# Optimization experiments

Hardware: AMD Instinct MI355X
Metric: run time of the kernel (lower is better)

## Reference

```python
import jax, jax.numpy as jnp
import numpy as np

B, T, Q, H = 128, 50, 1024, 256
MAX_STEP = 50
TEMP = 0.5
SUP_W, DIST_W, EMBED_W, LOSS_WEIGHT = 1.0, 0.01, 1.0, 1.0
BLUR, DIAMETER, REACH, SCALING, P = 0.005, 1.0, 500.0, 0.5, 2
NEG = -1e9


def _softmin(eps, C, h):
    # h: log-weights + potential/eps over the second axis of C
    return -eps * jax.nn.logsumexp(h[None, :] - C / eps, axis=1)


def _sqcost(u, v):
    sq = jnp.sum(u * u, -1)[:, None] + jnp.sum(v * v, -1)[None, :] - 2.0 * (u @ v.T)
    return 0.5 * jnp.maximum(sq, 0.0)  # geomloss p=2 cost: |x-y|^2 / 2


def sinkhorn_divergence(x, y):
    # geomloss SamplesLoss('sinkhorn', p=2, blur=0.005, diameter=1, reach=500),
    # tensorized, debiased, unbalanced, eps-scaling schedule.
    N, M = x.shape[0], y.shape[0]
    a_log = jnp.full((N,), -np.log(float(N)), dtype=x.dtype)
    b_log = jnp.full((M,), -np.log(float(M)), dtype=x.dtype)
    Cxy, Cyx = _sqcost(x, y), _sqcost(y, x)
    Cxx, Cyy = _sqcost(x, x), _sqcost(y, y)
    rho = REACH ** P
    eps_final = BLUR ** P
    eps_list = []
    e = DIAMETER ** P
    while e > eps_final:
        eps_list.append(e)
        e = e * (SCALING ** P)
    eps_list.append(eps_final)
    f_ab = jnp.zeros((N,), x.dtype)
    g_ab = jnp.zeros((M,), x.dtype)
    f_aa = jnp.zeros((N,), x.dtype)
    g_bb = jnp.zeros((M,), x.dtype)
    for eps in eps_list:  # static schedule (~9 steps)
        damp = 1.0 / (1.0 + eps / rho)
        ft = damp * _softmin(eps, Cxy, b_log + g_ab / eps)
        gt = damp * _softmin(eps, Cyx, a_log + f_ab / eps)
        faa = 0.5 * (f_aa + damp * _softmin(eps, Cxx, a_log + f_aa / eps))
        gbb = 0.5 * (g_bb + damp * _softmin(eps, Cyy, b_log + g_bb / eps))
        f_ab, g_ab, f_aa, g_bb = ft, gt, faa, gbb
    w = rho + eps_final / 2.0  # UnbalancedWeight
    a_w, b_w = jnp.exp(a_log), jnp.exp(b_log)
    return (jnp.sum(a_w * w * (jnp.exp(-f_aa / rho) - jnp.exp(-f_ab / rho)))
            + jnp.sum(b_w * w * (jnp.exp(-g_bb / rho) - jnp.exp(-g_ab / rho))))


def _forward(lc, lt, le, ltc, ltt, lte, ohs, oht, ods, odt, batch):
    p_c, p_t, p_e = lc / TEMP, lt / TEMP, le / TEMP
    q_c, q_t, q_e = ltc / TEMP, ltt / TEMP, lte / TEMP
    flat = lambda z: z.reshape(z.shape[0], -1)
    loss_kd = (sinkhorn_divergence(flat(p_c), flat(q_c))
               + sinkhorn_divergence(flat(p_t), flat(q_t))
               + sinkhorn_divergence(flat(p_e), flat(q_e)))
    S = MAX_STEP - 1
    delta = batch[:, :, :Q] + batch[:, :, Q:]  # [B,T,Q] question one-hots
    a = jnp.floor(((batch[:, :, :Q] - batch[:, :, Q:]).sum(-1) + 1.0) / 2.0)[:, 1:1 + S]  # [B,S] correctness
    dsh = delta[:, 1:1 + S]  # [B,S,Q]
    # diagonal of p[:S] @ delta[1:].T == per-step gather of next question's logit
    pc = jnp.einsum('bsq,bsq->bs', p_c[:, :S], dsh)
    pt = jnp.einsum('bsq,bsq->bs', p_t[:, :S], dsh)
    pe = jnp.einsum('bsq,bsq->bs', p_e[:, :S], dsh)
    idx = jnp.arange(S)
    last = jnp.max(jnp.where(pc > 0, idx[None, :], -1), axis=1)  # last i with pc[i] > 0
    L = jnp.where(last >= 0, last + 1, S)  # no break => keep full length
    mask = idx[None, :] < L[:, None]
    def ce(logits):
        m = jnp.where(mask, logits, NEG)
        lsm = m - jax.nn.logsumexp(m, axis=1, keepdims=True)
        return -jnp.sum(jnp.where(mask, a * lsm, 0.0))  # soft-target CE, summed over students
    loss_sup = ce(pt) + ce(pc) + ce(pe)
    embed = 0.5 * (jnp.sum((ohs - oht) ** 2) + jnp.sum((ods - odt) ** 2))
    total = LOSS_WEIGHT * (SUP_W * loss_sup + DIST_W * loss_kd + EMBED_W * embed)
    return total.reshape(1)


def setup_inputs():
    key = jax.random.key(0)
    ks = jax.random.split(key, 12)
    rn = lambda k, s: jax.random.normal(k, s, dtype=jnp.float32)
    qid = jax.random.randint(ks[10], (B, T), 0, Q)
    correct = jax.random.randint(ks[11], (B, T), 0, 2).astype(jnp.float32)
    oh = jax.nn.one_hot(qid, Q, dtype=jnp.float32)
    batch = jnp.concatenate([oh * correct[..., None], oh * (1.0 - correct)[..., None]], axis=-1)
    return {
        'logit_c': rn(ks[0], (B, T, Q)),
        'logit_t': rn(ks[1], (B, T, Q)),
        'logit_ensemble': rn(ks[2], (B, T, Q)),
        'logit_teacher_c': rn(ks[3], (B, T, Q)),
        'logit_teacher_t': rn(ks[4], (B, T, Q)),
        'logit_teacher_ensemble': rn(ks[5], (B, T, Q)),
        'out_h_student': rn(ks[6], (B, T, H)),
        'out_h_teacher': rn(ks[7], (B, T, H)),
        'out_d_student': rn(ks[8], (B, T, H)),
        'out_d_teacher': rn(ks[9], (B, T, H)),
        'batch': batch,
    }


def reference(logit_c, logit_t, logit_ensemble, logit_teacher_c, logit_teacher_t, logit_teacher_ensemble, out_h_student, out_h_teacher, out_d_student, out_d_teacher, batch):
    return _forward(logit_c, logit_t, logit_ensemble, logit_teacher_c, logit_teacher_t, logit_teacher_ensemble, out_h_student, out_h_teacher, out_d_student, out_d_teacher, batch)
```

## Files before the change

kernel.cpp:

```cpp
#include <hip/hip_runtime.h>

#define NB 128
#define T_DIM 50
#define Q_DIM 1024
#define H_DIM 256
#define S_DIM 49
#define K_DIM 51200
#define KCHUNKS 40
#define KC 1280
#define BK 64
#define GRAM_N (NB * NB)
#define LROWU 36

typedef __attribute__((ext_vector_type(4))) float f32x4;
typedef __attribute__((ext_vector_type(8))) _Float16 half8v;
typedef __attribute__((ext_vector_type(4))) unsigned int uint4v;
typedef __attribute__((ext_vector_type(2))) unsigned int uint2v;
using pk2_t = decltype(__builtin_amdgcn_cvt_pkrtz(0.0f, 0.0f));

union PKU { pk2_t p; unsigned int u; };
union U4H8 { uint4v u; half8v h; };

__device__ inline unsigned short f2bf(float x) {
  union { float f; unsigned int u; } v; v.f = x;
  return (unsigned short)(v.u >> 16);
}
__device__ inline float bf2f(unsigned short b) {
  union { float f; unsigned int u; } v; v.u = ((unsigned int)b) << 16;
  return v.f;
}

__global__ __launch_bounds__(512) void gram_tile_kernel(
    const float* __restrict__ s0, const float* __restrict__ s1, const float* __restrict__ s2,
    const float* __restrict__ t0, const float* __restrict__ t1, const float* __restrict__ t2,
    float* __restrict__ part) {
  __shared__ unsigned int panA[NB * LROWU];
  __shared__ unsigned int panB[NB * LROWU];

  const int g = blockIdx.y;
  const int pair = g / 3, kind = g % 3;
  const float* sp = (pair == 0) ? s0 : ((pair == 1) ? s1 : s2);
  const float* tp = (pair == 0) ? t0 : ((pair == 1) ? t1 : t2);
  const float* X = (kind == 2) ? tp : sp;
  const float* Y = (kind == 1) ? sp : tp;

  const int tid = threadIdx.x;
  const int wave = tid >> 6, lane = tid & 63;
  const int rhalf = wave >> 2, colq = wave & 3;
  const int l15 = lane & 15, quad = lane >> 4;

  f32x4 acc[4][2];
#pragma unroll
  for (int i = 0; i < 4; i++)
#pragma unroll
    for (int j = 0; j < 2; j++)
      acc[i][j] = (f32x4){0.f, 0.f, 0.f, 0.f};

  const int kbase = blockIdx.x * KC;
  for (int ks0 = 0; ks0 < KC; ks0 += BK) {
    __syncthreads();
#pragma unroll
    for (int m = 0; m < 2; m++) {
      const float* src = m ? Y : X;
      unsigned int* pan = m ? panB : panA;
#pragma unroll
      for (int i = 0; i < 4; i++) {
        const int f4 = tid + 512 * i;
        const int row = f4 >> 4, kq = f4 & 15;
        const f32x4 v = *(const f32x4*)(src + (size_t)row * K_DIM + (kbase + ks0 + kq * 4));
        PKU a, b;
        a.p = __builtin_amdgcn_cvt_pkrtz(v[0], v[1]);
        b.p = __builtin_amdgcn_cvt_pkrtz(v[2], v[3]);
        uint2v w; w.x = a.u; w.y = b.u;
        *(uint2v*)&pan[row * LROWU + kq * 2] = w;
      }
    }
    __syncthreads();
#pragma unroll
    for (int ks = 0; ks < 2; ks++) {
      half8v af[4], bf[2];
#pragma unroll
      for (int t = 0; t < 4; t++) {
        const int row = rhalf * 64 + t * 16 + l15;
        U4H8 u; u.u = *(const uint4v*)&panA[row * LROWU + ks * 16 + quad * 4];
        af[t] = u.h;
      }
#pragma unroll
      for (int t = 0; t < 2; t++) {
        const int row = colq * 32 + t * 16 + l15;
        U4H8 u; u.u = *(const uint4v*)&panB[row * LROWU + ks * 16 + quad * 4];
        bf[t] = u.h;
      }
#pragma unroll
      for (int ti = 0; ti < 4; ti++)
#pragma unroll
        for (int tj = 0; tj < 2; tj++)
          acc[ti][tj] = __builtin_amdgcn_mfma_f32_16x16x32_f16(af[ti], bf[tj], acc[ti][tj], 0, 0, 0);
    }
  }

  float* out = part + ((size_t)g * KCHUNKS + blockIdx.x) * GRAM_N;
#pragma unroll
  for (int ti = 0; ti < 4; ti++)
#pragma unroll
    for (int tj = 0; tj < 2; tj++)
#pragma unroll
      for (int r = 0; r < 4; r++) {
        const int row = rhalf * 64 + ti * 16 + quad * 4 + r;
        const int col = colq * 32 + tj * 16 + l15;
        out[(size_t)row * NB + col] = acc[ti][tj][r];
      }
}

__global__ __launch_bounds__(256) void gram_reduce_kernel(
    const float* __restrict__ part, float* __restrict__ gram) {
  const int idx = blockIdx.x * 256 + threadIdx.x;
  const int g = idx >> 14;
  const int cell = idx & (GRAM_N - 1);
  const float* p = part + (size_t)g * KCHUNKS * GRAM_N + cell;
  float s = 0.f;
#pragma unroll
  for (int c = 0; c < KCHUNKS; c++) s += p[(size_t)c * GRAM_N];
  gram[idx] = s;
}

__global__ __launch_bounds__(256) void sinkhorn_part_kernel(
    const float* __restrict__ gram, float* __restrict__ kdpart) {
  const int pair = blockIdx.x, kind = blockIdx.y;
  const float* Gxy = gram + (size_t)(3 * pair + 0) * GRAM_N;
  const float* Gxx = gram + (size_t)(3 * pair + 1) * GRAM_N;
  const float* Gyy = gram + (size_t)(3 * pair + 2) * GRAM_N;

  __shared__ unsigned short C[NB][132];
  __shared__ float nx[NB], ny[NB];
  __shared__ float pot0[NB], pot1[NB];
  __shared__ float np0[NB], np1[NB];
  __shared__ float red[256];

  const int tid = threadIdx.x;
  if (tid < NB) {
    nx[tid] = Gxx[tid * (NB + 1)];
    ny[tid] = Gyy[tid * (NB + 1)];
    pot0[tid] = 0.f; pot1[tid] = 0.f;
  }
  __syncthreads();

  const float* G  = (kind == 0) ? Gxy : ((kind == 1) ? Gxx : Gyy);
  const float* rn = (kind == 2) ? ny : nx;
  const float* cn = (kind == 1) ? nx : ny;
  for (int idx = tid; idx < GRAM_N; idx += 256) {
    const int i = idx >> 7, j = idx & 127;
    const float c = 2.0f * fmaxf(rn[i] + cn[j] - 2.0f * G[idx], 0.0f);
    C[i][j] = f2bf(c);
  }
  __syncthreads();

  const float rho = 250000.0f;
  const float AL = -4.852030263919617f;
  const int grp = tid >> 7;
  const int i = tid & 127;
  const bool active = (kind == 0) ? true : (grp == 0);
  const bool colread = (kind == 0) && (grp == 1);

  float eps = 1.0f;
  for (int it = 0; it < 9; it++) {
    if (it == 8) eps = 2.5e-5f;
    const float inv_eps = 1.0f / eps;
    const float damp = 1.0f / (1.0f + eps / rho);
    const float ebl = eps * AL;

    if (active) {
      const float* h = (kind == 0 && grp == 0) ? pot1 : pot0;
      float m0 = -3.0e38f, m1 = -3.0e38f, m2 = -3.0e38f, m3 = -3.0e38f;
      float s0 = 0.f, s1 = 0.f, s2 = 0.f, s3 = 0.f;
      for (int j = 0; j < NB; j += 4) {
        float c0, c1, c2, c3;
        if (colread) {
          c0 = bf2f(C[j + 0][i]); c1 = bf2f(C[j + 1][i]);
          c2 = bf2f(C[j + 2][i]); c3 = bf2f(C[j + 3][i]);
        } else {
          c0 = bf2f(C[i][j + 0]); c1 = bf2f(C[i][j + 1]);
          c2 = bf2f(C[i][j + 2]); c3 = bf2f(C[i][j + 3]);
        }
        const float u0 = ebl + h[j + 0] - c0;
        const float u1 = ebl + h[j + 1] - c1;
        const float u2 = ebl + h[j + 2] - c2;
        const float u3 = ebl + h[j + 3] - c3;
        float nm;
        nm = fmaxf(m0, u0); s0 = s0 * __expf((m0 - nm) * inv_eps) + __expf((u0 - nm) * inv_eps); m0 = nm;
        nm = fmaxf(m1, u1); s1 = s1 * __expf((m1 - nm) * inv_eps) + __expf((u1 - nm) * inv_eps); m1 = nm;
        nm = fmaxf(m2, u2); s2 = s2 * __expf((m2 - nm) * inv_eps) + __expf((u2 - nm) * inv_eps); m2 = nm;
        nm = fmaxf(m3, u3); s3 = s3 * __expf((m3 - nm) * inv_eps) + __expf((u3 - nm) * inv_eps); m3 = nm;
      }
      const float M = fmaxf(fmaxf(m0, m1), fmaxf(m2, m3));
      const float S = s0 * __expf((m0 - M) * inv_eps) + s1 * __expf((m1 - M) * inv_eps)
                    + s2 * __expf((m2 - M) * inv_eps) + s3 * __expf((m3 - M) * inv_eps);
      const float sm = -(M + eps * __logf(S));
      float newp;
      if (kind == 0) newp = damp * sm;
      else           newp = 0.5f * (pot0[i] + damp * sm);
      if (grp == 0) np0[i] = newp; else np1[i] = newp;
    }
    __syncthreads();
    if (tid < NB) {
      pot0[tid] = np0[tid];
      if (kind == 0) pot1[tid] = np1[tid];
    }
    __syncthreads();
    eps *= 0.25f;
  }

  float v = 0.f;
  if (kind == 0) {
    v = (grp == 0) ? -__expf(-pot0[i] / rho)
                   : -__expf(-pot1[i] / rho);
  } else if (grp == 0) {
    v = __expf(-pot0[i] / rho);
  }
  red[tid] = v;
  __syncthreads();
  for (int st = 128; st > 0; st >>= 1) {
    if (tid < st) red[tid] += red[tid + st];
    __syncthreads();
  }
  if (tid == 0) kdpart[pair * 3 + kind] = red[0];
}

__global__ __launch_bounds__(256) void ps_kernel(
    const float* __restrict__ lc, const float* __restrict__ lt, const float* __restrict__ le,
    const float* __restrict__ batch,
    float* __restrict__ pc, float* __restrict__ pt, float* __restrict__ pe,
    float* __restrict__ aarr) {
  const int bs = blockIdx.x;
  const int b = bs / S_DIM, s = bs % S_DIM;
  const float* brow = batch + ((size_t)b * T_DIM + (s + 1)) * (2 * Q_DIM);
  __shared__ int sq;
  __shared__ float sds;
  if (threadIdx.x == 0) sq = 0;
  __syncthreads();
  for (int q = threadIdx.x; q < Q_DIM; q += 256) {
    float d0 = brow[q], d1 = brow[Q_DIM + q];
    if (d0 + d1 > 0.5f) { sq = q; sds = d0 - d1; }
  }
  __syncthreads();
  if (threadIdx.x == 0) {
    const size_t off = ((size_t)b * T_DIM + s) * Q_DIM + sq;
    pc[bs] = 2.0f * lc[off];
    pt[bs] = 2.0f * lt[off];
    pe[bs] = 2.0f * le[off];
    aarr[bs] = (sds > 0.0f) ? 1.0f : 0.0f;
  }
}

__global__ __launch_bounds__(256) void embed_kernel(
    const f32x4* __restrict__ hs, const f32x4* __restrict__ ht,
    const f32x4* __restrict__ ds, const f32x4* __restrict__ dt,
    float* __restrict__ acc) {
  const int N4 = NB * T_DIM * H_DIM / 4;
  float sum = 0.f;
  for (int idx = blockIdx.x * 256 + threadIdx.x; idx < N4; idx += gridDim.x * 256) {
    f32x4 a = hs[idx] - ht[idx];
    f32x4 b = ds[idx] - dt[idx];
    sum += a[0]*a[0] + a[1]*a[1] + a[2]*a[2] + a[3]*a[3]
         + b[0]*b[0] + b[1]*b[1] + b[2]*b[2] + b[3]*b[3];
  }
  for (int off = 32; off > 0; off >>= 1) sum += __shfl_down(sum, off, 64);
  __shared__ float wsum[4];
  const int lane = threadIdx.x & 63, wv = threadIdx.x >> 6;
  if (lane == 0) wsum[wv] = sum;
  __syncthreads();
  if (threadIdx.x == 0) atomicAdd(acc, wsum[0] + wsum[1] + wsum[2] + wsum[3]);
}

__device__ inline float ce_row(const float* __restrict__ x, const float* __restrict__ a, int L) {
  float m = -3.0e38f;
  for (int s = 0; s < L; s++) m = fmaxf(m, x[s]);
  float sum = 0.f;
  for (int s = 0; s < L; s++) sum += __expf(x[s] - m);
  const float lse = m + __logf(sum);
  float loss = 0.f;
  for (int s = 0; s < L; s++) loss += a[s] * (x[s] - lse);
  return -loss;
}

__global__ __launch_bounds__(128) void ce_final_kernel(
    const float* __restrict__ pc, const float* __restrict__ pt, const float* __restrict__ pe,
    const float* __restrict__ aarr, const float* __restrict__ kdpart,
    const float* __restrict__ emb, float* __restrict__ out) {
  const int b = threadIdx.x;
  const float* xc = pc + b * S_DIM;
  const float* xt = pt + b * S_DIM;
  const float* xe = pe + b * S_DIM;
  const float* av = aarr + b * S_DIM;
  int last = -1;
  for (int s = 0; s < S_DIM; s++)
    if (xc[s] > 0.0f) last = s;
  const int L = (last >= 0) ? (last + 1) : S_DIM;
  float loss = ce_row(xt, av, L) + ce_row(xc, av, L) + ce_row(xe, av, L);
  __shared__ float red[128];
  red[b] = loss;
  __syncthreads();
  for (int st = 64; st > 0; st >>= 1) {
    if (b < st) red[b] += red[b + st];
    __syncthreads();
  }
  if (b == 0) {
    float kd = 0.f;
    for (int k = 0; k < 9; k++) kd += kdpart[k];
    out[0] = red[0] + 0.01f * (250000.0000125f / 128.0f) * kd + 0.5f * emb[0];
  }
}

extern "C" void kernel_launch(void* const* d_in, const int* in_sizes, int n_in,
                              void* d_out, int out_size, void* d_ws, size_t ws_size,
                              hipStream_t stream) {
  const float* lc    = (const float*)d_in[0];
  const float* lt    = (const float*)d_in[1];
  const float* le    = (const float*)d_in[2];
  const float* ltc   = (const float*)d_in[3];
  const float* ltt   = (const float*)d_in[4];
  const float* lte   = (const float*)d_in[5];
  const float* ohs   = (const float*)d_in[6];
  const float* oht   = (const float*)d_in[7];
  const float* ods   = (const float*)d_in[8];
  const float* odt   = (const float*)d_in[9];
  const float* batch = (const float*)d_in[10];

  float* ws   = (float*)d_ws;
  float* part = ws;
  float* gram = part + (size_t)9 * KCHUNKS * GRAM_N;
  float* pcb  = gram + 9 * GRAM_N;
  float* ptb  = pcb + NB * S_DIM;
  float* peb  = ptb + NB * S_DIM;
  float* ab   = peb + NB * S_DIM;
  float* kdp  = ab + NB * S_DIM;
  float* emb  = kdp + 9;

  hipMemsetAsync(emb, 0, sizeof(float), stream);

  embed_kernel<<<512, 256, 0, stream>>>(
      (const f32x4*)ohs, (const f32x4*)oht, (const f32x4*)ods, (const f32x4*)odt, emb);

  ps_kernel<<<NB * S_DIM, 256, 0, stream>>>(lc, lt, le, batch, pcb, ptb, peb, ab);

  gram_tile_kernel<<<dim3(KCHUNKS, 9), 512, 0, stream>>>(lc, lt, le, ltc, ltt, lte, part);

  gram_reduce_kernel<<<(9 * GRAM_N) / 256, 256, 0, stream>>>(part, gram);

  sinkhorn_part_kernel<<<dim3(3, 3), 256, 0, stream>>>(gram, kdp);

  ce_final_kernel<<<1, 128, 0, stream>>>(pcb, ptb, peb, ab, kdp, emb, (float*)d_out);
}
```

Measured before the change: 389.1 us.

## Fuse XY/XX/YY Gram tiles per pair and store bf16 partials

The Gram kernel now computes all three Gram matrices (XY, XX, YY) for a pair in one 1024-thread block. Each S and T panel is loaded from global memory once instead of being reloaded for each of the three kinds. It also doubles the number of K chunks, register-prefetches the next K slice while the current one is computed, and writes partial sums as rounded bf16 to halve partial-buffer traffic in the reduce. The risks are precision loss from summing 80 bf16 partials, and higher register pressure from three accumulator sets at 1024 threads.

After: 377.0 us. -3.1%, faster.

```diff
diff --git a/kernel.cpp b/kernel.cpp
--- a/kernel.cpp
+++ b/kernel.cpp
@@ -6,9 +6,10 @@
 #define H_DIM 256
 #define S_DIM 49
 #define K_DIM 51200
-#define KCHUNKS 40
-#define KC 1280
+#define KCHUNKS 80
+#define KC 640
 #define BK 64
+#define NSTAGE 10
 #define GRAM_N (NB * NB)
 #define LROWU 36
 
@@ -21,106 +22,138 @@
 union PKU { pk2_t p; unsigned int u; };
 union U4H8 { uint4v u; half8v h; };
 
-__device__ inline unsigned short f2bf(float x) {
+__device__ inline unsigned short f2bf_rn(float x) {
   union { float f; unsigned int u; } v; v.f = x;
-  return (unsigned short)(v.u >> 16);
+  unsigned int r = v.u + 0x7FFFu + ((v.u >> 16) & 1u);
+  return (unsigned short)(r >> 16);
 }
 __device__ inline float bf2f(unsigned short b) {
   union { float f; unsigned int u; } v; v.u = ((unsigned int)b) << 16;
   return v.f;
 }
 
-__global__ __launch_bounds__(512) void gram_tile_kernel(
+__global__ __launch_bounds__(1024) void gram_fused_kernel(
     const float* __restrict__ s0, const float* __restrict__ s1, const float* __restrict__ s2,
     const float* __restrict__ t0, const float* __restrict__ t1, const float* __restrict__ t2,
-    float* __restrict__ part) {
+    unsigned short* __restrict__ part) {
   __shared__ unsigned int panA[NB * LROWU];
   __shared__ unsigned int panB[NB * LROWU];
 
-  const int g = blockIdx.y;
-  const int pair = g / 3, kind = g % 3;
-  const float* sp = (pair == 0) ? s0 : ((pair == 1) ? s1 : s2);
-  const float* tp = (pair == 0) ? t0 : ((pair == 1) ? t1 : t2);
-  const float* X = (kind == 2) ? tp : sp;
-  const float* Y = (kind == 1) ? sp : tp;
+  const int chunk = blockIdx.x;
+  const int pair = blockIdx.y;
+  const float* S  = (pair == 0) ? s0 : ((pair == 1) ? s1 : s2);
+  const float* Tm = (pair == 0) ? t0 : ((pair == 1) ? t1 : t2);
 
   const int tid = threadIdx.x;
   const int wave = tid >> 6, lane = tid & 63;
-  const int rhalf = wave >> 2, colq = wave & 3;
+  const int wrow = wave >> 2, wcol = wave & 3;
   const int l15 = lane & 15, quad = lane >> 4;
 
-  f32x4 acc[4][2];
-#pragma unroll
-  for (int i = 0; i < 4; i++)
-#pragma unroll
-    for (int j = 0; j < 2; j++)
-      acc[i][j] = (f32x4){0.f, 0.f, 0.f, 0.f};
-
-  const int kbase = blockIdx.x * KC;
-  for (int ks0 = 0; ks0 < KC; ks0 += BK) {
-    __syncthreads();
-#pragma unroll
-    for (int m = 0; m < 2; m++) {
-      const float* src = m ? Y : X;
-      unsigned int* pan = m ? panB : panA;
-#pragma unroll
-      for (int i = 0; i < 4; i++) {
-        const int f4 = tid + 512 * i;
-        const int row = f4 >> 4, kq = f4 & 15;
-        const f32x4 v = *(const f32x4*)(src + (size_t)row * K_DIM + (kbase + ks0 + kq * 4));
-        PKU a, b;
-        a.p = __builtin_amdgcn_cvt_pkrtz(v[0], v[1]);
-        b.p = __builtin_amdgcn_cvt_pkrtz(v[2], v[3]);
-        uint2v w; w.x = a.u; w.y = b.u;
-        *(uint2v*)&pan[row * LROWU + kq * 2] = w;
+  f32x4 aXY[2][2], aXX[2][2], aYY[2][2];
+#pragma unroll
+  for (int i = 0; i < 2; i++)
+#pragma unroll
+    for (int j = 0; j < 2; j++) {
+      aXY[i][j] = (f32x4){0.f, 0.f, 0.f, 0.f};
+      aXX[i][j] = (f32x4){0.f, 0.f, 0.f, 0.f};
+      aYY[i][j] = (f32x4){0.f, 0.f, 0.f, 0.f};
+    }
+
+  const int r0 = tid >> 4;
+  const int kq = tid & 15;
+  const size_t ro0 = (size_t)r0 * K_DIM;
+  const size_t ro1 = (size_t)(r0 + 64) * K_DIM;
+
+  const int kbase = chunk * KC;
+  f32x4 pre0, pre1, pre2, pre3;
+
+#define ISSUE_LOADS(KPOS)                                    \
+  {                                                          \
+    const float* pS = S + (KPOS) + kq * 4;                   \
+    const float* pT = Tm + (KPOS) + kq * 4;                  \
+    pre0 = *(const f32x4*)(pS + ro0);                        \
+    pre1 = *(const f32x4*)(pS + ro1);                        \
+    pre2 = *(const f32x4*)(pT + ro0);                        \
+    pre3 = *(const f32x4*)(pT + ro1);                        \
+  }
+
+  ISSUE_LOADS(kbase)
+
+  for (int st = 0; st < NSTAGE; st++) {
+    if (st) __syncthreads();
+    {
+      PKU a, b; uint2v w;
+      a.p = __builtin_amdgcn_cvt_pkrtz(pre0[0], pre0[1]);
+      b.p = __builtin_amdgcn_cvt_pkrtz(pre0[2], pre0[3]);
+      w.x = a.u; w.y = b.u;
+      *(uint2v*)&panA[r0 * LROWU + kq * 2] = w;
+      a.p = __builtin_amdgcn_cvt_pkrtz(pre1[0], pre1[1]);
+      b.p = __builtin_amdgcn_cvt_pkrtz(pre1[2], pre1[3]);
+      w.x = a.u; w.y = b.u;
+      *(uint2v*)&panA[(r0 + 64) * LROWU + kq * 2] = w;
+      a.p = __builtin_amdgcn_cvt_pkrtz(pre2[0], pre2[1]);
+      b.p = __builtin_amdgcn_cvt_pkrtz(pre2[2], pre2[3]);
+      w.x = a.u; w.y = b.u;
+      *(uint2v*)&panB[r0 * LROWU + kq * 2] = w;
+      a.p = __builtin_amdgcn_cvt_pkrtz(pre3[0], pre3[1]);
+      b.p = __builtin_amdgcn_cvt_pkrtz(pre3[2], pre3[3]);
+      w.x = a.u; w.y = b.u;
+      *(uint2v*)&panB[(r0 + 64) * LROWU + kq * 2] = w;
+    }
+    __syncthreads();
+    if (st + 1 < NSTAGE) ISSUE_LOADS(kbase + (st + 1) * BK)
+
+#pragma unroll
+    for (int ks = 0; ks < 2; ks++) {
+      const int kc = ks * 16 + quad * 4;
+      half8v as_[2], bs_[2], at_[2], bt_[2];
+#pragma unroll
+      for (int t = 0; t < 2; t++) {
+        U4H8 u;
+        u.u = *(const uint4v*)&panA[(wrow * 32 + t * 16 + l15) * LROWU + kc]; as_[t] = u.h;
+        u.u = *(const uint4v*)&panA[(wcol * 32 + t * 16 + l15) * LROWU + kc]; bs_[t] = u.h;
+        u.u = *(const uint4v*)&panB[(wrow * 32 + t * 16 + l15) * LROWU + kc]; at_[t] = u.h;
+        u.u = *(const uint4v*)&panB[(wcol * 32 + t * 16 + l15) * LROWU + kc]; bt_[t] = u.h;
       }
-    }
-    __syncthreads();
-#pragma unroll
-    for (int ks = 0; ks < 2; ks++) {
-      half8v af[4], bf[2];
-#pragma unroll
-      for (int t = 0; t < 4; t++) {
-        const int row = rhalf * 64 + t * 16 + l15;
-        U4H8 u; u.u = *(const uint4v*)&panA[row * LROWU + ks * 16 + quad * 4];
-        af[t] = u.h;
+#pragma unroll
+      for (int ti = 0; ti < 2; ti++)
+#pragma unroll
+        for (int tj = 0; tj < 2; tj++) {
+          aXY[ti][tj] = __builtin_amdgcn_mfma_f32_16x16x32_f16(as_[ti], bt_[tj], aXY[ti][tj], 0, 0, 0);
+          aXX[ti][tj] = __builtin_amdgcn_mfma_f32_16x16x32_f16(as_[ti], bs_[tj], aXX[ti][tj], 0, 0, 0);
+          aYY[ti][tj] = __builtin_amdgcn_mfma_f32_16x16x32_f16(at_[ti], bt_[tj], aYY[ti][tj], 0, 0, 0);
+        }
+    }
+  }
+#undef ISSUE_LOADS
+
+#pragma unroll
+  for (int kind = 0; kind < 3; kind++) {
+    unsigned short* out = part + ((size_t)(pair * 3 + kind) * KCHUNKS + chunk) * GRAM_N;
+#pragma unroll
+    for (int ti = 0; ti < 2; ti++)
+#pragma unroll
+      for (int tj = 0; tj < 2; tj++) {
+        const f32x4 v = (kind == 0) ? aXY[ti][tj] : ((kind == 1) ? aXX[ti][tj] : aYY[ti][tj]);
+        const int col = wcol * 32 + tj * 16 + l15;
+#pragma unroll
+        for (int r = 0; r < 4; r++) {
+          const int row = wrow * 32 + ti * 16 + quad * 4 + r;
+          out[(size_t)row * NB + col] = f2bf_rn(v[r]);
+        }
       }
-#pragma unroll
-      for (int t = 0; t < 2; t++) {
-        const int row = colq * 32 + t * 16 + l15;
-        U4H8 u; u.u = *(const uint4v*)&panB[row * LROWU + ks * 16 + quad * 4];
-        bf[t] = u.h;
-      }
-#pragma unroll
-      for (int ti = 0; ti < 4; ti++)
-#pragma unroll
-        for (int tj = 0; tj < 2; tj++)
-          acc[ti][tj] = __builtin_amdgcn_mfma_f32_16x16x32_f16(af[ti], bf[tj], acc[ti][tj], 0, 0, 0);
-    }
-  }
-
-  float* out = part + ((size_t)g * KCHUNKS + blockIdx.x) * GRAM_N;
-#pragma unroll
-  for (int ti = 0; ti < 4; ti++)
-#pragma unroll
-    for (int tj = 0; tj < 2; tj++)
-#pragma unroll
-      for (int r = 0; r < 4; r++) {
-        const int row = rhalf * 64 + ti * 16 + quad * 4 + r;
-        const int col = colq * 32 + tj * 16 + l15;
-        out[(size_t)row * NB + col] = acc[ti][tj][r];
-      }
+  }
 }
 
 __global__ __launch_bounds__(256) void gram_reduce_kernel(
-    const float* __restrict__ part, float* __restrict__ gram) {
+    const unsigned short* __restrict__ part, float* __restrict__ gram) {
   const int idx = blockIdx.x * 256 + threadIdx.x;
   const int g = idx >> 14;
   const int cell = idx & (GRAM_N - 1);
-  const float* p = part + (size_t)g * KCHUNKS * GRAM_N + cell;
+  const unsigned short* p = part + (size_t)g * KCHUNKS * GRAM_N + cell;
   float s = 0.f;
 #pragma unroll
-  for (int c = 0; c < KCHUNKS; c++) s += p[(size_t)c * GRAM_N];
+  for (int c = 0; c < KCHUNKS; c++) s += bf2f(p[(size_t)c * GRAM_N]);
   gram[idx] = s;
 }
 
@@ -151,7 +184,7 @@
   for (int idx = tid; idx < GRAM_N; idx += 256) {
     const int i = idx >> 7, j = idx & 127;
     const float c = 2.0f * fmaxf(rn[i] + cn[j] - 2.0f * G[idx], 0.0f);
-    C[i][j] = f2bf(c);
+    C[i][j] = f2bf_rn(c);
   }
   __syncthreads();
 
@@ -193,9 +226,9 @@
         nm = fmaxf(m3, u3); s3 = s3 * __expf((m3 - nm) * inv_eps) + __expf((u3 - nm) * inv_eps); m3 = nm;
       }
       const float M = fmaxf(fmaxf(m0, m1), fmaxf(m2, m3));
-      const float S = s0 * __expf((m0 - M) * inv_eps) + s1 * __expf((m1 - M) * inv_eps)
-                    + s2 * __expf((m2 - M) * inv_eps) + s3 * __expf((m3 - M) * inv_eps);
-      const float sm = -(M + eps * __logf(S));
+      const float Ssum = s0 * __expf((m0 - M) * inv_eps) + s1 * __expf((m1 - M) * inv_eps)
+                       + s2 * __expf((m2 - M) * inv_eps) + s3 * __expf((m3 - M) * inv_eps);
+      const float sm = -(M + eps * __logf(Ssum));
       float newp;
       if (kind == 0) newp = damp * sm;
       else           newp = 0.5f * (pot0[i] + damp * sm);
@@ -326,9 +359,8 @@
   const float* odt   = (const float*)d_in[9];
   const float* batch = (const float*)d_in[10];
 
-  float* ws   = (float*)d_ws;
-  float* part = ws;
-  float* gram = part + (size_t)9 * KCHUNKS * GRAM_N;
+  unsigned short* part = (unsigned short*)d_ws;
+  float* gram = (float*)(part + (size_t)9 * KCHUNKS * GRAM_N);
   float* pcb  = gram + 9 * GRAM_N;
   float* ptb  = pcb + NB * S_DIM;
   float* peb  = ptb + NB * S_DIM;
@@ -343,7 +375,7 @@
 
   ps_kernel<<<NB * S_DIM, 256, 0, stream>>>(lc, lt, le, batch, pcb, ptb, peb, ab);
 
-  gram_tile_kernel<<<dim3(KCHUNKS, 9), 512, 0, stream>>>(lc, lt, le, ltc, ltt, lte, part);
+  gram_fused_kernel<<<dim3(KCHUNKS, 3), 1024, 0, stream>>>(lc, lt, le, ltc, ltt, lte, part);
 
   gram_reduce_kernel<<<(9 * GRAM_N) / 256, 256, 0, stream>>>(part, gram);
 
```
